# Kernel optimization log

Hardware: AMD Instinct MI355X
Metric: run time of the kernel (lower is better)

Reference implementation:

```python
import jax, jax.numpy as jnp
import numpy as np

K = 8  # in-edges per non-source node (forward direction)

def _mp_forward(y, src_local, pre_w, pre_b, upd_w, upd_b):
    # y: [L, P, D] node features by topological level; src_local: [L-1, P*K]
    L, P, D = y.shape
    # level 0 has no in-edges: builtin mean gives z = 0 -> y += relu(update(0)) = relu(b)
    y0 = jax.nn.relu(upd_b) + y[0]
    def step(y_prev, inp):
        src, y_init = inp
        msg = jax.nn.relu(y_prev[src] @ pre_w + pre_b)      # [P*K, D] gather + msg FNN
        z = msg.reshape(P, K, D).mean(axis=1)               # fn.mean reduce
        y_new = jax.nn.relu(z @ upd_w + upd_b) + y_init     # update + residual
        return y_new, y_new
    _, ys = jax.lax.scan(step, y0, (src_local, y[1:]))
    return jnp.concatenate([y0[None], ys], axis=0)

def _mp_reverse(y, src_local, pre_w, pre_b, upd_w, upd_b):
    # propagate along reversed edges, reverse topological order
    L, P, D = y.shape
    dst_local = jnp.repeat(jnp.arange(P), K)                # local dst of each fwd edge
    y_last = jax.nn.relu(upd_b) + y[-1]                     # sinks: z = 0
    def step(y_next, inp):
        src, y_init = inp
        msg = jax.nn.relu(y_next[dst_local] @ pre_w + pre_b)            # [P*K, D]
        z_sum = jax.ops.segment_sum(msg, src, num_segments=P)
        deg = jax.ops.segment_sum(jnp.ones((P * K,), msg.dtype), src, num_segments=P)
        z = z_sum / jnp.maximum(deg, 1.0)[:, None]          # mean; zero-deg -> 0
        y_new = jax.nn.relu(z @ upd_w + upd_b) + y_init
        return y_new, y_new
    _, ys = jax.lax.scan(step, y_last, (src_local, y[:-1]), reverse=True)
    return jnp.concatenate([ys, y_last[None]], axis=0)

def setup_inputs() -> dict:
    key = jax.random.key(0)
    ks = jax.random.split(key, 16)
    N, node_dim, D = 131072, 128, 128   # D = out_dim // 2
    L, P = 16, 8192
    s = 0.06
    return {
        "x": jax.random.normal(ks[0], (N, node_dim), jnp.float32),
        "src_local": jax.random.randint(ks[1], (L - 1, P * K), 0, P).astype(jnp.int32),
        "nt_w1": jax.random.normal(ks[2], (node_dim, node_dim), jnp.float32) * s,
        "nt_b1": jax.random.normal(ks[3], (node_dim,), jnp.float32) * s,
        "nt_w2": jax.random.normal(ks[4], (node_dim, D), jnp.float32) * s,
        "nt_b2": jax.random.normal(ks[5], (D,), jnp.float32) * s,
        "f_pre_w": jax.random.normal(ks[6], (D, D), jnp.float32) * s,
        "f_pre_b": jax.random.normal(ks[7], (D,), jnp.float32) * s,
        "f_upd_w": jax.random.normal(ks[8], (D, D), jnp.float32) * s,
        "f_upd_b": jax.random.normal(ks[9], (D,), jnp.float32) * s,
        "b_pre_w": jax.random.normal(ks[10], (D, D), jnp.float32) * s,
        "b_pre_b": jax.random.normal(ks[11], (D,), jnp.float32) * s,
        "b_upd_w": jax.random.normal(ks[12], (D, D), jnp.float32) * s,
        "b_upd_b": jax.random.normal(ks[13], (D,), jnp.float32) * s,
    }

def reference(x, src_local, nt_w1, nt_b1, nt_w2, nt_b2,
              f_pre_w, f_pre_b, f_upd_w, f_upd_b,
              b_pre_w, b_pre_b, b_upd_w, b_upd_b):
    Lm1, PK = src_local.shape
    P, L = PK // K, Lm1 + 1
    N = x.shape[0]
    # node_transform: FNN(node_dim, [node_dim], out_dim//2)
    h = jax.nn.relu(x @ nt_w1 + nt_b1) @ nt_w2 + nt_b2      # [N, D]
    y = h.reshape(L, P, -1)
    hf = _mp_forward(y, src_local, f_pre_w, f_pre_b, f_upd_w, f_upd_b).reshape(N, -1)
    hb = _mp_reverse(y, src_local, b_pre_w, b_pre_b, b_upd_w, b_upd_b).reshape(N, -1)
    return jnp.concatenate([hf, hb], axis=1)
```

## Files before the change

### kernel.cpp

```cpp
#include <hip/hip_runtime.h>
#include <cstddef>
#include <cstdint>

#define DD   128
#define PP   8192
#define KK   8
#define LLV  16
#define NN   131072
#define NE   65536
#define NLVL 15

typedef _Float16 h8 __attribute__((ext_vector_type(8)));
typedef _Float16 h4 __attribute__((ext_vector_type(4)));
typedef float f4v __attribute__((ext_vector_type(4)));

__device__ __forceinline__ float4 ld4(const float* p) { return *(const float4*)p; }
__device__ __forceinline__ void st4(float* p, float4 v) { *(float4*)p = v; }

__device__ __forceinline__ int swz(int row, int k) { return row * 128 + (k ^ ((row & 7) << 3)); }
__device__ __forceinline__ int uswz(int row, int c) { return row * 128 + (c ^ ((row & 7) << 2)); }

__device__ __forceinline__ void split_store(_Float16* ah, _Float16* al, int row, int k0, float4 v) {
  int o = swz(row, k0);
  h4 hi, lo;
  _Float16 t0 = (_Float16)v.x; hi[0] = t0; lo[0] = (_Float16)(v.x - (float)t0);
  _Float16 t1 = (_Float16)v.y; hi[1] = t1; lo[1] = (_Float16)(v.y - (float)t1);
  _Float16 t2 = (_Float16)v.z; hi[2] = t2; lo[2] = (_Float16)(v.z - (float)t2);
  _Float16 t3 = (_Float16)v.w; hi[3] = t3; lo[3] = (_Float16)(v.w - (float)t3);
  *(h4*)(ah + o) = hi;
  *(h4*)(al + o) = lo;
}

__device__ __forceinline__ void load_bfrags1(const _Float16* __restrict__ img, int t16, int lane,
                                             h8 Bh[4], h8 Bl[4]) {
#pragma unroll
  for (int ks = 0; ks < 4; ks++) {
    int o = ((t16 * 4 + ks) * 64 + lane) * 8;
    Bh[ks] = *(const h8*)(img + o);
    Bl[ks] = *(const h8*)(img + 16384 + o);
  }
}

__device__ __forceinline__ f4v gemm_rt(const _Float16* __restrict__ ah, const _Float16* __restrict__ al,
                                       const h8 Bh[4], const h8 Bl[4], int rbase, int lane) {
  int r16 = lane & 15, kb = lane >> 4;
  int arow = rbase + r16;
  h8 Ah[4], Al[4];
#pragma unroll
  for (int ks = 0; ks < 4; ks++) {
    int o = swz(arow, ks * 32 + kb * 8);
    Ah[ks] = *(const h8*)(ah + o);
    Al[ks] = *(const h8*)(al + o);
  }
  f4v a = {0.f, 0.f, 0.f, 0.f};
#pragma unroll
  for (int ks = 0; ks < 4; ks++) a = __builtin_amdgcn_mfma_f32_16x16x32_f16(Ah[ks], Bh[ks], a, 0, 0, 0);
#pragma unroll
  for (int ks = 0; ks < 4; ks++) a = __builtin_amdgcn_mfma_f32_16x16x32_f16(Al[ks], Bh[ks], a, 0, 0, 0);
#pragma unroll
  for (int ks = 0; ks < 4; ks++) a = __builtin_amdgcn_mfma_f32_16x16x32_f16(Ah[ks], Bl[ks], a, 0, 0, 0);
  return a;
}

__global__ __launch_bounds__(256) void prep_all(
    const float* __restrict__ w0, const float* __restrict__ w1,
    const float* __restrict__ w2, const float* __restrict__ w3,
    const float* __restrict__ w4, const float* __restrict__ w5,
    _Float16* __restrict__ img_base) {
  int mat = blockIdx.x >> 3;
  int g = (blockIdx.x & 7) * 256 + threadIdx.x;
  const float* w;
  switch (mat) {
    case 0: w = w0; break;
    case 1: w = w1; break;
    case 2: w = w2; break;
    case 3: w = w3; break;
    case 4: w = w4; break;
    default: w = w5; break;
  }
  _Float16* img = img_base + (size_t)mat * 32768;
  int t16 = g >> 8, ks = (g >> 6) & 3, lane = g & 63;
  int n = t16 * 16 + (lane & 15);
  int kb = ks * 32 + (lane >> 4) * 8;
  h8 hi, lo;
#pragma unroll
  for (int j = 0; j < 8; j++) {
    float v = w[(kb + j) * 128 + n];
    _Float16 h = (_Float16)v;
    hi[j] = h;
    lo[j] = (_Float16)(v - (float)h);
  }
  int o = ((t16 * 4 + ks) * 64 + lane) * 8;
  *(h8*)(img + o) = hi;
  *(h8*)(img + 16384 + o) = lo;
}

__global__ __launch_bounds__(512, 4) void nt_kernel(
    const float* __restrict__ x,
    const _Float16* __restrict__ w1img, const float* __restrict__ b1,
    const _Float16* __restrict__ w2img, const float* __restrict__ b2,
    float* __restrict__ hout) {
  __shared__ __align__(16) _Float16 asplit[16384];
  __shared__ __align__(16) float dbuf[8192];
  _Float16* ah = asplit;
  _Float16* al = asplit + 8192;
  int tid = threadIdx.x;
  int lane = tid & 63, wv = tid >> 6;
  int c4 = tid & 31, rg4 = (tid >> 5) * 4;
  size_t base = (size_t)blockIdx.x * 64;

  h8 Bh[4], Bl[4];
  load_bfrags1(w1img, wv, lane, Bh, Bl);

#pragma unroll
  for (int j = 0; j < 4; j++) {
    int s = tid + j * 512;
    float4 v = ((const float4*)(x + base * 128))[s];
    split_store(ah, al, s >> 5, (s & 31) * 4, v);
  }
  __syncthreads();

  f4v acc[4];
#pragma unroll
  for (int rt = 0; rt < 4; rt++) acc[rt] = gemm_rt(ah, al, Bh, Bl, rt * 16, lane);
  {
    int r16 = lane & 15, kb = lane >> 4;
    int col = wv * 16 + r16;
    float b = b1[col];
#pragma unroll
    for (int rt = 0; rt < 4; rt++)
#pragma unroll
      for (int r = 0; r < 4; r++)
        dbuf[uswz(rt * 16 + kb * 4 + r, col)] = fmaxf(acc[rt][r] + b, 0.f);
  }
  load_bfrags1(w2img, wv, lane, Bh, Bl);
  __syncthreads();

  float4 uu[4];
#pragma unroll
  for (int i = 0; i < 4; i++) uu[i] = *(const float4*)(dbuf + uswz(rg4 + i, c4 * 4));
#pragma unroll
  for (int i = 0; i < 4; i++) split_store(ah, al, rg4 + i, c4 * 4, uu[i]);
  __syncthreads();

#pragma unroll
  for (int rt = 0; rt < 4; rt++) acc[rt] = gemm_rt(ah, al, Bh, Bl, rt * 16, lane);
  {
    int r16 = lane & 15, kb = lane >> 4;
    int col = wv * 16 + r16;
    float b = b2[col];
#pragma unroll
    for (int rt = 0; rt < 4; rt++)
#pragma unroll
      for (int r = 0; r < 4; r++)
        dbuf[uswz(rt * 16 + kb * 4 + r, col)] = acc[rt][r] + b;
  }
  __syncthreads();
#pragma unroll
  for (int i = 0; i < 4; i++)
    st4(hout + (base + rg4 + i) * 128 + c4 * 4, *(const float4*)(dbuf + uswz(rg4 + i, c4 * 4)));
}

__global__ __launch_bounds__(256) void csr_count(const int* __restrict__ src_all,
                                                 int* __restrict__ deg) {
  int e = blockIdx.x * 256 + threadIdx.x;
  int l = e >> 16;
  int q = src_all[e];
  atomicAdd(&deg[l * PP + q], 1);
}

__global__ __launch_bounds__(256) void csr_scan(const int* __restrict__ deg,
                                                int* __restrict__ offs,
                                                int* __restrict__ cursor) {
  int l = blockIdx.x;
  int t = threadIdx.x;
  const int* d = deg + l * PP;
  __shared__ int ssum[256];
  int loc[32];
  int s = 0;
#pragma unroll
  for (int j = 0; j < 32; j++) { loc[j] = d[t * 32 + j]; s += loc[j]; }
  ssum[t] = s;
  __syncthreads();
  for (int off = 1; off < 256; off <<= 1) {
    int v = (t >= off) ? ssum[t - off] : 0;
    __syncthreads();
    ssum[t] += v;
    __syncthreads();
  }
  int run = (t == 0) ? 0 : ssum[t - 1];
#pragma unroll
  for (int j = 0; j < 32; j++) {
    offs[l * (PP + 1) + t * 32 + j] = run;
    cursor[l * PP + t * 32 + j] = run;
    run += loc[j];
  }
  if (t == 255) offs[l * (PP + 1) + PP] = run;
}

__global__ __launch_bounds__(256) void csr_fill(const int* __restrict__ src_all,
                                                int* __restrict__ cursor,
                                                int* __restrict__ edges) {
  int e = blockIdx.x * 256 + threadIdx.x;
  int l = e >> 16;
  int q = src_all[e];
  int pos = atomicAdd(&cursor[l * PP + q], 1);
  edges[l * NE + pos] = (e & (NE - 1)) >> 3;
}

__global__ __launch_bounds__(512, 4) void mp_step(
    const float* __restrict__ h,
    const int* __restrict__ src_all,
    const int* __restrict__ offs,
    const int* __restrict__ edges,
    const _Float16* __restrict__ fw_upd_img, const float* __restrict__ fw_upd_b,
    const _Float16* __restrict__ fw_pre_img, const float* __restrict__ fw_pre_b,
    const _Float16* __restrict__ bw_upd_img, const float* __restrict__ bw_upd_b,
    const _Float16* __restrict__ bw_pre_img, const float* __restrict__ bw_pre_b,
    const _Float16* __restrict__ mf_in, _Float16* __restrict__ mf_out,
    const _Float16* __restrict__ mb_in, _Float16* __restrict__ mb_out,
    float* __restrict__ out, int step) {
  __shared__ __align__(16) _Float16 asplit[8192];
  __shared__ __align__(16) float dbuf[4096];
  _Float16* ah = asplit;
  _Float16* al = asplit + 4096;
  int tid = threadIdx.x;
  int lane = tid & 63, wv = tid >> 6;
  int c4 = tid & 31, rg2 = (tid >> 5) * 2;
  bool is_fwd = blockIdx.x < 256;
  int tile = (blockIdx.x & 255) * 32;
  int level = is_fwd ? step : 15 - step;
  const _Float16* upd_img = is_fwd ? fw_upd_img : bw_upd_img;
  const float* upd_b = is_fwd ? fw_upd_b : bw_upd_b;
  const _Float16* pre_img = is_fwd ? fw_pre_img : bw_pre_img;
  const float* pre_b = is_fwd ? fw_pre_b : bw_pre_b;
  const _Float16* m_in = is_fwd ? mf_in : mb_in;
  _Float16* m_out      = is_fwd ? mf_out : mb_out;
  bool has_mout = (step < 15);
  int col_off = is_fwd ? 0 : 128;

  float4 res[2];
#pragma unroll
  for (int i = 0; i < 2; i++) {
    int n = level * PP + tile + rg2 + i;
    res[i] = ld4(h + (size_t)n * 128 + c4 * 4);
  }

  float4 u[2];
  if (step == 0) {
    float4 bv = ld4(upd_b + c4 * 4);
    float4 rb;
    rb.x = fmaxf(bv.x, 0.f); rb.y = fmaxf(bv.y, 0.f);
    rb.z = fmaxf(bv.z, 0.f); rb.w = fmaxf(bv.w, 0.f);
#pragma unroll
    for (int i = 0; i < 2; i++) {
      u[i].x = rb.x + res[i].x; u[i].y = rb.y + res[i].y;
      u[i].z = rb.z + res[i].z; u[i].w = rb.w + res[i].w;
    }
  } else {
    h8 BhU[4], BlU[4];
    load_bfrags1(upd_img, wv, lane, BhU, BlU);

    if (is_fwd) {
      const int* src = src_all + (step - 1) * NE;
#pragma unroll
      for (int i = 0; i < 2; i++) {
        int r = rg2 + i;
        int p = tile + r;
        h4 v[8];
#pragma unroll
        for (int k = 0; k < 8; k++) {
          int sidx = src[p * 8 + k];
          v[k] = *(const h4*)(m_in + (size_t)sidx * 128 + c4 * 4);
        }
        float4 a;
        a.x = (((float)v[0][0] + (float)v[1][0]) + ((float)v[2][0] + (float)v[3][0])) +
              (((float)v[4][0] + (float)v[5][0]) + ((float)v[6][0] + (float)v[7][0]));
        a.y = (((float)v[0][1] + (float)v[1][1]) + ((float)v[2][1] + (float)v[3][1])) +
              (((float)v[4][1] + (float)v[5][1]) + ((float)v[6][1] + (float)v[7][1]));
        a.z = (((float)v[0][2] + (float)v[1][2]) + ((float)v[2][2] + (float)v[3][2])) +
              (((float)v[4][2] + (float)v[5][2]) + ((float)v[6][2] + (float)v[7][2]));
        a.w = (((float)v[0][3] + (float)v[1][3]) + ((float)v[2][3] + (float)v[3][3])) +
              (((float)v[4][3] + (float)v[5][3]) + ((float)v[6][3] + (float)v[7][3]));
        a.x *= 0.125f; a.y *= 0.125f; a.z *= 0.125f; a.w *= 0.125f;
        split_store(ah, al, r, c4 * 4, a);
      }
    } else {
      const int* off_l = offs + level * (PP + 1);
      const int* ep = edges + level * NE;
#pragma unroll
      for (int i = 0; i < 2; i++) {
        int r = rg2 + i;
        int q = tile + r;
        int e0 = off_l[q], e1 = off_l[q + 1];
        float4 a = {0.f, 0.f, 0.f, 0.f};
        int idx = e0;
        for (; idx + 4 <= e1; idx += 4) {
          int p0 = ep[idx], p1 = ep[idx + 1], p2 = ep[idx + 2], p3 = ep[idx + 3];
          h4 v0 = *(const h4*)(m_in + (size_t)p0 * 128 + c4 * 4);
          h4 v1 = *(const h4*)(m_in + (size_t)p1 * 128 + c4 * 4);
          h4 v2 = *(const h4*)(m_in + (size_t)p2 * 128 + c4 * 4);
          h4 v3 = *(const h4*)(m_in + (size_t)p3 * 128 + c4 * 4);
          a.x += ((float)v0[0] + (float)v1[0]) + ((float)v2[0] + (float)v3[0]);
          a.y += ((float)v0[1] + (float)v1[1]) + ((float)v2[1] + (float)v3[1]);
          a.z += ((float)v0[2] + (float)v1[2]) + ((float)v2[2] + (float)v3[2]);
          a.w += ((float)v0[3] + (float)v1[3]) + ((float)v2[3] + (float)v3[3]);
        }
        for (; idx < e1; idx++) {
          int p = ep[idx];
          h4 v = *(const h4*)(m_in + (size_t)p * 128 + c4 * 4);
          a.x += (float)v[0]; a.y += (float)v[1]; a.z += (float)v[2]; a.w += (float)v[3];
        }
        float inv = (e1 > e0) ? 1.0f / (float)(e1 - e0) : 0.f;
        a.x *= inv; a.y *= inv; a.z *= inv; a.w *= inv;
        split_store(ah, al, r, c4 * 4, a);
      }
    }
    __syncthreads();

    f4v acc[2];
#pragma unroll
    for (int rt = 0; rt < 2; rt++) acc[rt] = gemm_rt(ah, al, BhU, BlU, rt * 16, lane);
    {
      int r16 = lane & 15, kb = lane >> 4;
      int col = wv * 16 + r16;
      float b = upd_b[col];
#pragma unroll
      for (int rt = 0; rt < 2; rt++)
#pragma unroll
        for (int r = 0; r < 4; r++)
          dbuf[uswz(rt * 16 + kb * 4 + r, col)] = fmaxf(acc[rt][r] + b, 0.f);
    }
    __syncthreads();

#pragma unroll
    for (int i = 0; i < 2; i++) {
      int r = rg2 + i;
      float4 uv = *(const float4*)(dbuf + uswz(r, c4 * 4));
      u[i].x = uv.x + res[i].x;
      u[i].y = uv.y + res[i].y;
      u[i].z = uv.z + res[i].z;
      u[i].w = uv.w + res[i].w;
    }
  }

#pragma unroll
  for (int i = 0; i < 2; i++) {
    int n = level * PP + tile + rg2 + i;
    st4(out + (size_t)n * 256 + col_off + c4 * 4, u[i]);
  }

  if (has_mout) {
    h8 BhP[4], BlP[4];
    load_bfrags1(pre_img, wv, lane, BhP, BlP);
#pragma unroll
    for (int i = 0; i < 2; i++) split_store(ah, al, rg2 + i, c4 * 4, u[i]);
    __syncthreads();
    f4v acc[2];
#pragma unroll
    for (int rt = 0; rt < 2; rt++) acc[rt] = gemm_rt(ah, al, BhP, BlP, rt * 16, lane);
    {
      int r16 = lane & 15, kb = lane >> 4;
      int col = wv * 16 + r16;
      float b = pre_b[col];
#pragma unroll
      for (int rt = 0; rt < 2; rt++)
#pragma unroll
        for (int r = 0; r < 4; r++)
          dbuf[uswz(rt * 16 + kb * 4 + r, col)] = fmaxf(acc[rt][r] + b, 0.f);
    }
    __syncthreads();
#pragma unroll
    for (int i = 0; i < 2; i++) {
      int r = rg2 + i;
      float4 m = *(const float4*)(dbuf + uswz(r, c4 * 4));
      h4 mh;
      mh[0] = (_Float16)m.x; mh[1] = (_Float16)m.y;
      mh[2] = (_Float16)m.z; mh[3] = (_Float16)m.w;
      *(h4*)(m_out + (size_t)(tile + r) * 128 + c4 * 4) = mh;
    }
  }
}

extern "C" void kernel_launch(void* const* d_in, const int* in_sizes, int n_in,
                              void* d_out, int out_size, void* d_ws, size_t ws_size,
                              hipStream_t stream) {
  const float* x      = (const float*)d_in[0];
  const int*   src    = (const int*)d_in[1];
  const float* nt_w1  = (const float*)d_in[2];
  const float* nt_b1  = (const float*)d_in[3];
  const float* nt_w2  = (const float*)d_in[4];
  const float* nt_b2  = (const float*)d_in[5];
  const float* f_pre_w = (const float*)d_in[6];
  const float* f_pre_b = (const float*)d_in[7];
  const float* f_upd_w = (const float*)d_in[8];
  const float* f_upd_b = (const float*)d_in[9];
  const float* b_pre_w = (const float*)d_in[10];
  const float* b_pre_b = (const float*)d_in[11];
  const float* b_upd_w = (const float*)d_in[12];
  const float* b_upd_b = (const float*)d_in[13];
  float* out = (float*)d_out;

  float* wsf = (float*)d_ws;
  float* h   = wsf;
  _Float16* mf0 = (_Float16*)(h + (size_t)NN * DD);
  _Float16* mf1 = mf0 + (size_t)PP * DD;
  _Float16* mb0 = mf1 + (size_t)PP * DD;
  _Float16* mb1 = mb0 + (size_t)PP * DD;
  int* deg    = (int*)(mb1 + (size_t)PP * DD);
  int* offs   = deg + NLVL * PP;
  int* cursor = offs + NLVL * (PP + 1);
  int* edges  = cursor + NLVL * PP;

  uintptr_t ip = (uintptr_t)(edges + (size_t)NLVL * NE);
  ip = (ip + 15) & ~(uintptr_t)15;
  _Float16* img = (_Float16*)ip;
  _Float16* i_ntw1 = img;
  _Float16* i_ntw2 = img + 32768;
  _Float16* i_fupd = img + 2 * 32768;
  _Float16* i_fpre = img + 3 * 32768;
  _Float16* i_bupd = img + 4 * 32768;
  _Float16* i_bpre = img + 5 * 32768;

  hipMemsetAsync(deg, 0, (size_t)NLVL * PP * sizeof(int), stream);
  prep_all<<<48, 256, 0, stream>>>(nt_w1, nt_w2, f_upd_w, f_pre_w, b_upd_w, b_pre_w, img);

  csr_count<<<NLVL * NE / 256, 256, 0, stream>>>(src, deg);
  csr_scan<<<NLVL, 256, 0, stream>>>(deg, offs, cursor);
  csr_fill<<<NLVL * NE / 256, 256, 0, stream>>>(src, cursor, edges);
  nt_kernel<<<NN / 64, 512, 0, stream>>>(x, i_ntw1, nt_b1, i_ntw2, nt_b2, h);

  for (int s = 0; s < 16; s++) {
    const _Float16* mf_in = (s & 1) ? mf0 : mf1;
    _Float16* mf_out      = (s & 1) ? mf1 : mf0;
    const _Float16* mb_in = (s & 1) ? mb0 : mb1;
    _Float16* mb_out      = (s & 1) ? mb1 : mb0;
    mp_step<<<512, 512, 0, stream>>>(h, src, offs, edges,
                                     i_fupd, f_upd_b, i_fpre, f_pre_b,
                                     i_bupd, b_upd_b, i_bpre, b_pre_b,
                                     mf_in, mf_out, mb_in, mb_out, out, s);
  }
}
```

Baseline: 569.5 us.

## Drop activation low-half split in GEMMs and fuse CSR build into one setup kernel

Activations are now stored only as fp16, with no hi/lo split, so each GEMM tile issues two MFMA passes (A·Bh + A·Bl) instead of three, and the A-side shared-memory buffers are halved. The weight split is kept. Separately, the memset, weight prep, CSR count, scan and fill launches are merged into one kernel: blocks 12..26 each build one level's CSR using shared-memory atomics instead of global ones. The precision change adds roughly fp16-level rounding error on activations, and CSR edge order within a node remains nondeterministic.

```diff
diff --git a/kernel.cpp b/kernel.cpp
--- a/kernel.cpp
+++ b/kernel.cpp
@@ -20,15 +20,12 @@
 __device__ __forceinline__ int swz(int row, int k) { return row * 128 + (k ^ ((row & 7) << 3)); }
 __device__ __forceinline__ int uswz(int row, int c) { return row * 128 + (c ^ ((row & 7) << 2)); }
 
-__device__ __forceinline__ void split_store(_Float16* ah, _Float16* al, int row, int k0, float4 v) {
+__device__ __forceinline__ void hstore4(_Float16* ah, int row, int k0, float4 v) {
   int o = swz(row, k0);
-  h4 hi, lo;
-  _Float16 t0 = (_Float16)v.x; hi[0] = t0; lo[0] = (_Float16)(v.x - (float)t0);
-  _Float16 t1 = (_Float16)v.y; hi[1] = t1; lo[1] = (_Float16)(v.y - (float)t1);
-  _Float16 t2 = (_Float16)v.z; hi[2] = t2; lo[2] = (_Float16)(v.z - (float)t2);
-  _Float16 t3 = (_Float16)v.w; hi[3] = t3; lo[3] = (_Float16)(v.w - (float)t3);
+  h4 hi;
+  hi[0] = (_Float16)v.x; hi[1] = (_Float16)v.y;
+  hi[2] = (_Float16)v.z; hi[3] = (_Float16)v.w;
   *(h4*)(ah + o) = hi;
-  *(h4*)(al + o) = lo;
 }
 
 __device__ __forceinline__ void load_bfrags1(const _Float16* __restrict__ img, int t16, int lane,
@@ -41,58 +38,99 @@
   }
 }
 
-__device__ __forceinline__ f4v gemm_rt(const _Float16* __restrict__ ah, const _Float16* __restrict__ al,
+__device__ __forceinline__ f4v gemm_rt(const _Float16* __restrict__ ah,
                                        const h8 Bh[4], const h8 Bl[4], int rbase, int lane) {
   int r16 = lane & 15, kb = lane >> 4;
   int arow = rbase + r16;
-  h8 Ah[4], Al[4];
-#pragma unroll
-  for (int ks = 0; ks < 4; ks++) {
-    int o = swz(arow, ks * 32 + kb * 8);
-    Ah[ks] = *(const h8*)(ah + o);
-    Al[ks] = *(const h8*)(al + o);
-  }
+  h8 Ah[4];
+#pragma unroll
+  for (int ks = 0; ks < 4; ks++) Ah[ks] = *(const h8*)(ah + swz(arow, ks * 32 + kb * 8));
   f4v a = {0.f, 0.f, 0.f, 0.f};
 #pragma unroll
   for (int ks = 0; ks < 4; ks++) a = __builtin_amdgcn_mfma_f32_16x16x32_f16(Ah[ks], Bh[ks], a, 0, 0, 0);
-#pragma unroll
-  for (int ks = 0; ks < 4; ks++) a = __builtin_amdgcn_mfma_f32_16x16x32_f16(Al[ks], Bh[ks], a, 0, 0, 0);
 #pragma unroll
   for (int ks = 0; ks < 4; ks++) a = __builtin_amdgcn_mfma_f32_16x16x32_f16(Ah[ks], Bl[ks], a, 0, 0, 0);
   return a;
 }
 
-__global__ __launch_bounds__(256) void prep_all(
+__global__ __launch_bounds__(1024) void setup_kernel(
     const float* __restrict__ w0, const float* __restrict__ w1,
     const float* __restrict__ w2, const float* __restrict__ w3,
     const float* __restrict__ w4, const float* __restrict__ w5,
-    _Float16* __restrict__ img_base) {
-  int mat = blockIdx.x >> 3;
-  int g = (blockIdx.x & 7) * 256 + threadIdx.x;
-  const float* w;
-  switch (mat) {
-    case 0: w = w0; break;
-    case 1: w = w1; break;
-    case 2: w = w2; break;
-    case 3: w = w3; break;
-    case 4: w = w4; break;
-    default: w = w5; break;
-  }
-  _Float16* img = img_base + (size_t)mat * 32768;
-  int t16 = g >> 8, ks = (g >> 6) & 3, lane = g & 63;
-  int n = t16 * 16 + (lane & 15);
-  int kb = ks * 32 + (lane >> 4) * 8;
-  h8 hi, lo;
-#pragma unroll
-  for (int j = 0; j < 8; j++) {
-    float v = w[(kb + j) * 128 + n];
-    _Float16 h = (_Float16)v;
-    hi[j] = h;
-    lo[j] = (_Float16)(v - (float)h);
-  }
-  int o = ((t16 * 4 + ks) * 64 + lane) * 8;
-  *(h8*)(img + o) = hi;
-  *(h8*)(img + 16384 + o) = lo;
+    _Float16* __restrict__ img_base,
+    const int* __restrict__ src_all,
+    int* __restrict__ offs, int* __restrict__ edges) {
+  int t = threadIdx.x;
+  if (blockIdx.x < 12) {
+    int mat = blockIdx.x >> 1;
+    int g = (blockIdx.x & 1) * 1024 + t;
+    const float* w;
+    switch (mat) {
+      case 0: w = w0; break;
+      case 1: w = w1; break;
+      case 2: w = w2; break;
+      case 3: w = w3; break;
+      case 4: w = w4; break;
+      default: w = w5; break;
+    }
+    _Float16* img = img_base + (size_t)mat * 32768;
+    int t16 = g >> 8, ks = (g >> 6) & 3, lane = g & 63;
+    int n = t16 * 16 + (lane & 15);
+    int kb = ks * 32 + (lane >> 4) * 8;
+    h8 hi, lo;
+#pragma unroll
+    for (int j = 0; j < 8; j++) {
+      float v = w[(kb + j) * 128 + n];
+      _Float16 h = (_Float16)v;
+      hi[j] = h;
+      lo[j] = (_Float16)(v - (float)h);
+    }
+    int o = ((t16 * 4 + ks) * 64 + lane) * 8;
+    *(h8*)(img + o) = hi;
+    *(h8*)(img + 16384 + o) = lo;
+  } else {
+    int l = blockIdx.x - 12;
+    const int* src = src_all + (size_t)l * NE;
+    __shared__ int cnt[PP];
+    __shared__ int bsum[1024];
+#pragma unroll
+    for (int j = 0; j < 8; j++) cnt[t + j * 1024] = 0;
+    __syncthreads();
+#pragma unroll 4
+    for (int j = 0; j < 64; j++) {
+      int q = src[j * 1024 + t];
+      atomicAdd(&cnt[q], 1);
+    }
+    __syncthreads();
+    int loc[8];
+    int s = 0;
+#pragma unroll
+    for (int j = 0; j < 8; j++) { loc[j] = cnt[t * 8 + j]; s += loc[j]; }
+    bsum[t] = s;
+    __syncthreads();
+    for (int off = 1; off < 1024; off <<= 1) {
+      int v = (t >= off) ? bsum[t - off] : 0;
+      __syncthreads();
+      bsum[t] += v;
+      __syncthreads();
+    }
+    int run = (t == 0) ? 0 : bsum[t - 1];
+#pragma unroll
+    for (int j = 0; j < 8; j++) {
+      offs[l * (PP + 1) + t * 8 + j] = run;
+      cnt[t * 8 + j] = run;
+      run += loc[j];
+    }
+    if (t == 1023) offs[l * (PP + 1) + PP] = run;
+    __syncthreads();
+#pragma unroll 4
+    for (int j = 0; j < 64; j++) {
+      int e = j * 1024 + t;
+      int q = src[e];
+      int pos = atomicAdd(&cnt[q], 1);
+      edges[(size_t)l * NE + pos] = e >> 3;
+    }
+  }
 }
 
 __global__ __launch_bounds__(512, 4) void nt_kernel(
@@ -100,10 +138,8 @@
     const _Float16* __restrict__ w1img, const float* __restrict__ b1,
     const _Float16* __restrict__ w2img, const float* __restrict__ b2,
     float* __restrict__ hout) {
-  __shared__ __align__(16) _Float16 asplit[16384];
+  __shared__ __align__(16) _Float16 abuf[8192];
   __shared__ __align__(16) float dbuf[8192];
-  _Float16* ah = asplit;
-  _Float16* al = asplit + 8192;
   int tid = threadIdx.x;
   int lane = tid & 63, wv = tid >> 6;
   int c4 = tid & 31, rg4 = (tid >> 5) * 4;
@@ -116,13 +152,13 @@
   for (int j = 0; j < 4; j++) {
     int s = tid + j * 512;
     float4 v = ((const float4*)(x + base * 128))[s];
-    split_store(ah, al, s >> 5, (s & 31) * 4, v);
+    hstore4(abuf, s >> 5, (s & 31) * 4, v);
   }
   __syncthreads();
 
   f4v acc[4];
 #pragma unroll
-  for (int rt = 0; rt < 4; rt++) acc[rt] = gemm_rt(ah, al, Bh, Bl, rt * 16, lane);
+  for (int rt = 0; rt < 4; rt++) acc[rt] = gemm_rt(abuf, Bh, Bl, rt * 16, lane);
   {
     int r16 = lane & 15, kb = lane >> 4;
     int col = wv * 16 + r16;
@@ -140,11 +176,11 @@
 #pragma unroll
   for (int i = 0; i < 4; i++) uu[i] = *(const float4*)(dbuf + uswz(rg4 + i, c4 * 4));
 #pragma unroll
-  for (int i = 0; i < 4; i++) split_store(ah, al, rg4 + i, c4 * 4, uu[i]);
+  for (int i = 0; i < 4; i++) hstore4(abuf, rg4 + i, c4 * 4, uu[i]);
   __syncthreads();
 
 #pragma unroll
-  for (int rt = 0; rt < 4; rt++) acc[rt] = gemm_rt(ah, al, Bh, Bl, rt * 16, lane);
+  for (int rt = 0; rt < 4; rt++) acc[rt] = gemm_rt(abuf, Bh, Bl, rt * 16, lane);
   {
     int r16 = lane & 15, kb = lane >> 4;
     int col = wv * 16 + r16;
@@ -159,53 +195,6 @@
 #pragma unroll
   for (int i = 0; i < 4; i++)
     st4(hout + (base + rg4 + i) * 128 + c4 * 4, *(const float4*)(dbuf + uswz(rg4 + i, c4 * 4)));
-}
-
-__global__ __launch_bounds__(256) void csr_count(const int* __restrict__ src_all,
-                                                 int* __restrict__ deg) {
-  int e = blockIdx.x * 256 + threadIdx.x;
-  int l = e >> 16;
-  int q = src_all[e];
-  atomicAdd(&deg[l * PP + q], 1);
-}
-
-__global__ __launch_bounds__(256) void csr_scan(const int* __restrict__ deg,
-                                                int* __restrict__ offs,
-                                                int* __restrict__ cursor) {
-  int l = blockIdx.x;
-  int t = threadIdx.x;
-  const int* d = deg + l * PP;
-  __shared__ int ssum[256];
-  int loc[32];
-  int s = 0;
-#pragma unroll
-  for (int j = 0; j < 32; j++) { loc[j] = d[t * 32 + j]; s += loc[j]; }
-  ssum[t] = s;
-  __syncthreads();
-  for (int off = 1; off < 256; off <<= 1) {
-    int v = (t >= off) ? ssum[t - off] : 0;
-    __syncthreads();
-    ssum[t] += v;
-    __syncthreads();
-  }
-  int run = (t == 0) ? 0 : ssum[t - 1];
-#pragma unroll
-  for (int j = 0; j < 32; j++) {
-    offs[l * (PP + 1) + t * 32 + j] = run;
-    cursor[l * PP + t * 32 + j] = run;
-    run += loc[j];
-  }
-  if (t == 255) offs[l * (PP + 1) + PP] = run;
-}
-
-__global__ __launch_bounds__(256) void csr_fill(const int* __restrict__ src_all,
-                                                int* __restrict__ cursor,
-                                                int* __restrict__ edges) {
-  int e = blockIdx.x * 256 + threadIdx.x;
-  int l = e >> 16;
-  int q = src_all[e];
-  int pos = atomicAdd(&cursor[l * PP + q], 1);
-  edges[l * NE + pos] = (e & (NE - 1)) >> 3;
 }
 
 __global__ __launch_bounds__(512, 4) void mp_step(
@@ -220,10 +209,8 @@
     const _Float16* __restrict__ mf_in, _Float16* __restrict__ mf_out,
     const _Float16* __restrict__ mb_in, _Float16* __restrict__ mb_out,
     float* __restrict__ out, int step) {
-  __shared__ __align__(16) _Float16 asplit[8192];
+  __shared__ __align__(16) _Float16 abuf[4096];
   __shared__ __align__(16) float dbuf[4096];
-  _Float16* ah = asplit;
-  _Float16* al = asplit + 4096;
   int tid = threadIdx.x;
   int lane = tid & 63, wv = tid >> 6;
   int c4 = tid & 31, rg2 = (tid >> 5) * 2;
@@ -283,7 +270,7 @@
         a.w = (((float)v[0][3] + (float)v[1][3]) + ((float)v[2][3] + (float)v[3][3])) +
               (((float)v[4][3] + (float)v[5][3]) + ((float)v[6][3] + (float)v[7][3]));
         a.x *= 0.125f; a.y *= 0.125f; a.z *= 0.125f; a.w *= 0.125f;
-        split_store(ah, al, r, c4 * 4, a);
+        hstore4(abuf, r, c4 * 4, a);
       }
     } else {
       const int* off_l = offs + level * (PP + 1);
@@ -313,14 +300,14 @@
         }
         float inv = (e1 > e0) ? 1.0f / (float)(e1 - e0) : 0.f;
         a.x *= inv; a.y *= inv; a.z *= inv; a.w *= inv;
-        split_store(ah, al, r, c4 * 4, a);
+        hstore4(abuf, r, c4 * 4, a);
       }
     }
     __syncthreads();
 
     f4v acc[2];
 #pragma unroll
-    for (int rt = 0; rt < 2; rt++) acc[rt] = gemm_rt(ah, al, BhU, BlU, rt * 16, lane);
+    for (int rt = 0; rt < 2; rt++) acc[rt] = gemm_rt(abuf, BhU, BlU, rt * 16, lane);
     {
       int r16 = lane & 15, kb = lane >> 4;
       int col = wv * 16 + r16;
@@ -354,11 +341,11 @@
     h8 BhP[4], BlP[4];
     load_bfrags1(pre_img, wv, lane, BhP, BlP);
 #pragma unroll
-    for (int i = 0; i < 2; i++) split_store(ah, al, rg2 + i, c4 * 4, u[i]);
+    for (int i = 0; i < 2; i++) hstore4(abuf, rg2 + i, c4 * 4, u[i]);
     __syncthreads();
     f4v acc[2];
 #pragma unroll
-    for (int rt = 0; rt < 2; rt++) acc[rt] = gemm_rt(ah, al, BhP, BlP, rt * 16, lane);
+    for (int rt = 0; rt < 2; rt++) acc[rt] = gemm_rt(abuf, BhP, BlP, rt * 16, lane);
     {
       int r16 = lane & 15, kb = lane >> 4;
       int col = wv * 16 + r16;
@@ -407,10 +394,8 @@
   _Float16* mf1 = mf0 + (size_t)PP * DD;
   _Float16* mb0 = mf1 + (size_t)PP * DD;
   _Float16* mb1 = mb0 + (size_t)PP * DD;
-  int* deg    = (int*)(mb1 + (size_t)PP * DD);
-  int* offs   = deg + NLVL * PP;
-  int* cursor = offs + NLVL * (PP + 1);
-  int* edges  = cursor + NLVL * PP;
+  int* offs   = (int*)(mb1 + (size_t)PP * DD);
+  int* edges  = offs + NLVL * (PP + 1);
 
   uintptr_t ip = (uintptr_t)(edges + (size_t)NLVL * NE);
   ip = (ip + 15) & ~(uintptr_t)15;
@@ -422,12 +407,8 @@
   _Float16* i_bupd = img + 4 * 32768;
   _Float16* i_bpre = img + 5 * 32768;
 
-  hipMemsetAsync(deg, 0, (size_t)NLVL * PP * sizeof(int), stream);
-  prep_all<<<48, 256, 0, stream>>>(nt_w1, nt_w2, f_upd_w, f_pre_w, b_upd_w, b_pre_w, img);
-
-  csr_count<<<NLVL * NE / 256, 256, 0, stream>>>(src, deg);
-  csr_scan<<<NLVL, 256, 0, stream>>>(deg, offs, cursor);
-  csr_fill<<<NLVL * NE / 256, 256, 0, stream>>>(src, cursor, edges);
+  setup_kernel<<<27, 1024, 0, stream>>>(nt_w1, nt_w2, f_upd_w, f_pre_w, b_upd_w, b_pre_w,
+                                        img, src, offs, edges);
   nt_kernel<<<NN / 64, 512, 0, stream>>>(x, i_ntw1, nt_b1, i_ntw2, nt_b2, h);
 
   for (int s = 0; s < 16; s++) {
```

Result: faster. 536.5 us (-5.8%).
